# Kernel tuning notes

Measured on AMD Instinct MI355X. Metric: run time of the kernel, lower is better.

Reference implementation:

```python
import jax, jax.numpy as jnp
import numpy as np

N, D, NUM_CLASSES = 8192, 128, 128
ALPHA = 1.0
K = 16


def setup_inputs() -> dict:
    key = jax.random.key(0)
    k1, k2 = jax.random.split(key)
    inputs = jax.random.normal(k1, (N, D), dtype=jnp.float32)
    targets = jax.random.randint(k2, (N,), 0, NUM_CLASSES, dtype=jnp.int64)
    return {"inputs": inputs, "targets": targets}


def knn_softmax(inputs, targets, alpha=ALPHA, k=K):
    n = inputs.shape[0]
    # pairwise euclidean distances (GEMM-based), clamped like the original
    sq = jnp.sum(inputs * inputs, axis=1)                      # [n]
    d2 = sq[:, None] + sq[None, :] - 2.0 * (inputs @ inputs.T)  # [n,n]
    dist = jnp.sqrt(jnp.maximum(d2, 1e-12))

    eye = jnp.eye(n, dtype=bool)
    same = targets[:, None] == targets[None, :]
    pos_mask = same & ~eye          # same label, off-diagonal
    neg_mask = ~same                # different label (diagonal excluded automatically)

    # per-row threshold: (K+1)-th smallest off-diagonal distance
    dm = jnp.where(eye, jnp.inf, dist)
    neg_topk, _ = jax.lax.top_k(-dm, k + 1)   # k+1 smallest (negated)
    thr = -neg_topk[:, k]                      # [n]

    below = dist < thr[:, None]
    pos_sel = pos_mask & below
    neg_sel = neg_mask & below

    exp_d = jnp.exp(-alpha * dist)
    pos_logit = jnp.sum(jnp.where(pos_sel, exp_d, 0.0), axis=1)  # [n]
    neg_logit = jnp.sum(jnp.where(neg_sel, exp_d, 0.0), axis=1)  # [n]
    count_pos = jnp.sum(pos_sel, axis=1)
    count_neg = jnp.sum(neg_sel, axis=1)

    # fallback when no positive falls below the threshold: use the first positive pair
    first_pos = jnp.argmax(pos_mask, axis=1)                     # [n]
    fb_dist = jnp.take_along_axis(dist, first_pos[:, None], axis=1)[:, 0]
    fallback = jnp.exp(-alpha * fb_dist)
    pos_eff = jnp.where(count_pos == 0, fallback, pos_logit)

    # rows with no positives or no negatives at all are skipped (`continue`)
    valid = pos_mask.any(axis=1) & neg_mask.any(axis=1)

    loss_i = -jnp.log(pos_eff / (pos_eff + neg_logit))
    loss = jnp.sum(jnp.where(valid, loss_i, 0.0)) / n

    count_pos_acc = jnp.where(count_pos == 0, 1, count_pos)  # fallback gives len 1
    accuracy = jnp.sum((valid & (count_pos_acc > count_neg)).astype(jnp.float32)) / n
    tp = jnp.sum(jnp.where(valid, count_pos, 0)).astype(jnp.float32) / n
    tn = jnp.sum(jnp.where(valid, count_neg, 0)).astype(jnp.float32) / n
    return loss, accuracy, tp, tn


def reference(inputs, targets):
    return knn_softmax(inputs, targets)
```

## Files before the change

kernel.cpp:

```cpp
#include <hip/hip_runtime.h>

#define NPTS 8192
#define DIM 128
#define NCLS 128
#define KSEL 17
#define RB   64
#define NT8  64
#define CAPW 40
#define SEG  32
#define NSEG 8
#define MBLK 1024
#define BIG 3.0e38f

typedef short bf16x8 __attribute__((ext_vector_type(8)));
typedef float f32x4 __attribute__((ext_vector_type(4)));

__device__ __forceinline__ unsigned short f2bf(float f) {
  unsigned int u = __float_as_uint(f);
  u += 0x7fffu + ((u >> 16) & 1u);
  return (unsigned short)(u >> 16);
}

__device__ __forceinline__ unsigned flipF(float f) {
  unsigned u = __float_as_uint(f);
  return (u & 0x80000000u) ? ~u : (u | 0x80000000u);
}
__device__ __forceinline__ float unflipF(unsigned k) {
  unsigned u = (k & 0x80000000u) ? (k & 0x7fffffffu) : ~k;
  return __uint_as_float(u);
}

__device__ __forceinline__ float kth17_4(float a, float b, float c, float d) {
  const unsigned ka = flipF(a), kb = flipF(b), kc = flipF(c), kd = flipF(d);
  unsigned ans = 0x80000000u;
  for (int bit = 30; bit >= 0; --bit) {
    unsigned mid = ans | (1u << bit);
    int cc = __popcll(__ballot(ka < mid)) + __popcll(__ballot(kb < mid)) +
             __popcll(__ballot(kc < mid)) + __popcll(__ballot(kd < mid));
    if (cc < KSEL) ans = mid;
  }
  return unflipF(ans);
}

__global__ void prep(const float* __restrict__ X, const long long* __restrict__ targets,
                     unsigned short* __restrict__ Xb, float* __restrict__ sqv,
                     int* __restrict__ tgt, int* __restrict__ ccount,
                     int* __restrict__ j0a, int* __restrict__ j1a) {
  const int tid = threadIdx.x;
  if (blockIdx.x == 2048) {
    __shared__ int cc[NCLS], c0[NCLS], c1[NCLS];
    if (tid < NCLS) { cc[tid] = 0; c0[tid] = 0x7fffffff; c1[tid] = 0x7fffffff; }
    __syncthreads();
    for (int base = tid * 4; base < NPTS; base += 1024) {
      const long long* p = targets + base;
#pragma unroll
      for (int k = 0; k < 4; k++) {
        int c = (int)p[k];
        tgt[base + k] = c;
        atomicAdd(&cc[c], 1);
        atomicMin(&c0[c], base + k);
      }
    }
    __syncthreads();
    for (int base = tid * 4; base < NPTS; base += 1024) {
#pragma unroll
      for (int k = 0; k < 4; k++) {
        int c = tgt[base + k];
        if (base + k != c0[c]) atomicMin(&c1[c], base + k);
      }
    }
    __syncthreads();
    if (tid < NCLS) { ccount[tid] = cc[tid]; j0a[tid] = c0[tid]; j1a[tid] = c1[tid]; }
    return;
  }
  const int w = tid >> 6, lane = tid & 63;
  const int gw = blockIdx.x * 4 + w;
  const float* xr = X + (size_t)gw * DIM;
  float a = xr[lane], b = xr[lane + 64];
  Xb[(size_t)gw * DIM + lane] = f2bf(a);
  Xb[(size_t)gw * DIM + lane + 64] = f2bf(b);
  float s = a * a + b * b;
#pragma unroll
  for (int off = 32; off; off >>= 1) s += __shfl_xor(s, off);
  if (lane == 0) sqv[gw] = s;
}

__global__ __launch_bounds__(256, 4) void knn_main(
    const unsigned short* __restrict__ Xb, const float* __restrict__ sqv,
    const int* __restrict__ tgt, float* __restrict__ scr, int* __restrict__ cscr) {
  __shared__ __align__(16) unsigned short shB[2][2048];
  __shared__ __align__(16) float shPub[RB * 64];
  __shared__ int cntL[RB];

  const int tid = threadIdx.x;
  const int w = tid >> 6;
  const int lane = tid & 63;
  const int quad = lane >> 4;
  const int l16 = lane & 15;
  const int rg = blockIdx.x >> 3;
  const int eighth = blockIdx.x & 7;
  const int rbase = rg * RB;
  const int cbase = eighth * 1024;

  const int swoff = (tid << 4) ^ (((tid >> 4) & 7) << 4);
  const unsigned lmlt = (1u << l16) - 1;
  int rdoff[4];
#pragma unroll
  for (int kb = 0; kb < 4; kb++)
    rdoff[kb] = (l16 * 256 + quad * 16 + kb * 64) ^ ((l16 & 7) << 4);

  bf16x8 afrag[4];
  {
    const unsigned short* arow = Xb + (size_t)(rbase + w * 16 + l16) * DIM + quad * 8;
#pragma unroll
    for (int kb = 0; kb < 4; kb++) afrag[kb] = *(const bf16x8*)(arow + kb * 32);
  }
  float sqi[4]; int ti[4];
#pragma unroll
  for (int r = 0; r < 4; r++) {
    int rr = rbase + w * 16 + quad * 4 + r;
    sqi[r] = sqv[rr]; ti[r] = tgt[rr];
  }
  int tdw;
  {
    int d = rbase + w * 16 - cbase;
    tdw = (d >= 0 && d < 1024) ? (d >> 4) : -1;
  }

  const unsigned short* gtile0 = Xb + (size_t)cbase * DIM;
  const float* sqp = sqv + cbase + l16;
  const int*   tgp = tgt + cbase + l16;

  float m1[4], m2[4], m3[4], m4[4];
#pragma unroll
  for (int r = 0; r < 4; r++) { m1[r] = BIG; m2[r] = BIG; m3[r] = BIG; m4[r] = BIG; }
  {
    bf16x8 s0 = *(const bf16x8*)(gtile0 + tid * 8);
    *(bf16x8*)((char*)&shB[0][0] + swoff) = s0;
  }
  float sqc = sqp[0];
  __syncthreads();
  for (int t = 0; t < NT8; t++) {
    const int tn = (t + 1) & (NT8 - 1);
    bf16x8 stg = *(const bf16x8*)(gtile0 + (size_t)tn * 2048 + tid * 8);
    const float sqn = sqp[tn * 16];
    const char* lb = (const char*)&shB[t & 1][0];
    bf16x8 b[4];
#pragma unroll
    for (int kb = 0; kb < 4; kb++) b[kb] = *(const bf16x8*)(lb + rdoff[kb]);
    f32x4 acc = {0.f, 0.f, 0.f, 0.f};
#pragma unroll
    for (int kb = 0; kb < 4; kb++)
      acc = __builtin_amdgcn_mfma_f32_16x16x32_bf16(afrag[kb], b[kb], acc, 0, 0, 0);
    float v[4];
#pragma unroll
    for (int r = 0; r < 4; r++) v[r] = fmaf(-2.0f, acc[r], sqc);
    if (t == tdw) {
#pragma unroll
      for (int r = 0; r < 4; r++) if (l16 == quad * 4 + r) v[r] = BIG;
    }
#pragma unroll
    for (int r = 0; r < 4; r++) {
      m4[r] = fminf(m4[r], fmaxf(m3[r], v[r]));
      m3[r] = fminf(m3[r], fmaxf(m2[r], v[r]));
      m2[r] = fminf(m2[r], fmaxf(m1[r], v[r]));
      m1[r] = fminf(m1[r], v[r]);
    }
    sqc = sqn;
    *(bf16x8*)((char*)&shB[(t & 1) ^ 1][0] + swoff) = stg;
    __syncthreads();
  }

#pragma unroll
  for (int r = 0; r < 4; r++) {
    f32x4 mq = {m1[r], m2[r], m3[r], m4[r]};
    *(f32x4*)&shPub[(w * 16 + quad * 4 + r) * 64 + l16 * 4] = mq;
  }
  __syncthreads();
  float Ur[4] = {0.f, 0.f, 0.f, 0.f};
  for (int rp = 0; rp < 16; rp += 2) {
    const unsigned ka = flipF(shPub[(w * 16 + rp) * 64 + lane]);
    const unsigned kb2 = flipF(shPub[(w * 16 + rp + 1) * 64 + lane]);
    unsigned ansA = 0u, ansB = 0u;
    for (int bit = 31; bit >= 14; --bit) {
      const unsigned mA = ansA | (1u << bit), mB = ansB | (1u << bit);
      const int ca = __popcll(__ballot(ka < mA));
      const int cb = __popcll(__ballot(kb2 < mB));
      if (ca < KSEL) ansA = mA;
      if (cb < KSEL) ansB = mB;
    }
    const float ua = unflipF(ansA | 0x3FFFu), ub = unflipF(ansB | 0x3FFFu);
#pragma unroll
    for (int r = 0; r < 4; r++) {
      const int myrow = quad * 4 + r;
      if (myrow == rp) Ur[r] = ua;
      if (myrow == rp + 1) Ur[r] = ub;
    }
  }

  float* bufD = shPub;
  int cntr[4] = {0, 0, 0, 0};
  {
    bf16x8 s0 = *(const bf16x8*)(gtile0 + tid * 8);
    *(bf16x8*)((char*)&shB[0][0] + swoff) = s0;
  }
  sqc = sqp[0];
  int tjc = tgp[0];
  __syncthreads();
  for (int t = 0; t < NT8; t++) {
    const int tn = (t + 1) & (NT8 - 1);
    bf16x8 stg = *(const bf16x8*)(gtile0 + (size_t)tn * 2048 + tid * 8);
    const float sqn = sqp[tn * 16];
    const int tjn = tgp[tn * 16];
    const char* lb = (const char*)&shB[t & 1][0];
    bf16x8 b[4];
#pragma unroll
    for (int kb = 0; kb < 4; kb++) b[kb] = *(const bf16x8*)(lb + rdoff[kb]);
    f32x4 acc = {0.f, 0.f, 0.f, 0.f};
#pragma unroll
    for (int kb = 0; kb < 4; kb++)
      acc = __builtin_amdgcn_mfma_f32_16x16x32_bf16(afrag[kb], b[kb], acc, 0, 0, 0);
    float v[4];
#pragma unroll
    for (int r = 0; r < 4; r++) v[r] = fmaf(-2.0f, acc[r], sqc);
    if (t == tdw) {
#pragma unroll
      for (int r = 0; r < 4; r++) if (l16 == quad * 4 + r) v[r] = BIG;
    }
#pragma unroll
    for (int r = 0; r < 4; r++) {
      const bool pred = (v[r] <= Ur[r]);
      const unsigned long long bal = __ballot(pred);
      if (bal) {
        const unsigned qm = (unsigned)(bal >> (quad << 4)) & 0xFFFFu;
        const int pos = cntr[r] + __popc(qm & lmlt);
        if (pred && pos < CAPW) {
          unsigned enc = __float_as_uint(fmaxf(v[r] + sqi[r], 0.0f));
          if (tjc == ti[r]) enc |= 0x80000000u;
          bufD[(w * 16 + quad * 4 + r) * CAPW + pos] = __uint_as_float(enc);
        }
        cntr[r] += __popc(qm);
      }
    }
    sqc = sqn; tjc = tjn;
    *(bf16x8*)((char*)&shB[(t & 1) ^ 1][0] + swoff) = stg;
    __syncthreads();
  }
#pragma unroll
  for (int r = 0; r < 4; r++)
    if (l16 == 0) cntL[w * 16 + quad * 4 + r] = cntr[r];
  __syncthreads();

  for (int rl = 0; rl < 16; rl++) {
    const int grow = rbase + w * 16 + rl;
    const int tot = cntL[w * 16 + rl];
    float* srow = scr + (size_t)grow * (NSEG * SEG) + eighth * SEG;
    if (tot <= SEG) {
      if (lane < tot) srow[lane] = bufD[(w * 16 + rl) * CAPW + lane];
      if (lane == 0) cscr[grow * NSEG + eighth] = tot;
    } else {
      const int n = min(tot, CAPW);
      float e = BIG; int m = 0;
      if (lane < n) {
        unsigned u = __float_as_uint(bufD[(w * 16 + rl) * CAPW + lane]);
        m = (int)(u >> 31); e = __uint_as_float(u & 0x7fffffffu);
      }
      for (int round = 0; round < KSEL; round++) {
        float vv = e; int idx = lane;
#pragma unroll
        for (int off = 32; off; off >>= 1) {
          float ov = __shfl_xor(vv, off);
          int   oi = __shfl_xor(idx, off);
          if (ov < vv || (ov == vv && oi < idx)) { vv = ov; idx = oi; }
        }
        if (idx == lane) {
          unsigned ub = __float_as_uint(e);
          if (m) ub |= 0x80000000u;
          srow[round] = __uint_as_float(ub);
          e = BIG;
        }
      }
      if (lane == 0) cscr[grow * NSEG + eighth] = KSEL;
    }
  }
}

__global__ __launch_bounds__(256) void knn_merge(
    const float* __restrict__ scr, const int* __restrict__ cscr,
    const float* __restrict__ sqv, const int* __restrict__ tgt,
    const int* __restrict__ ccount, const int* __restrict__ j0a,
    const int* __restrict__ j1a, const float* __restrict__ X32,
    float* __restrict__ pacc) {
  __shared__ float blockAcc[4];
  const int tid = threadIdx.x;
  const int w = tid >> 6;
  const int lane = tid & 63;
  if (tid < 4) blockAcc[tid] = 0.0f;
  __syncthreads();
  for (int ri = 0; ri < 2; ri++) {
    const int grow = blockIdx.x * 8 + w * 2 + ri;
    const float* srow = scr + (size_t)grow * (NSEG * SEG);
    const int h = lane >> 5, li = lane & 31;
    float e[4]; int mm[4];
#pragma unroll
    for (int j = 0; j < 4; j++) {
      const int seg = j * 2 + h;
      const int cj = cscr[grow * NSEG + seg];
      if (li < cj) {
        unsigned u = __float_as_uint(srow[seg * SEG + li]);
        mm[j] = (int)(u >> 31); e[j] = __uint_as_float(u & 0x7fffffffu);
      } else { e[j] = BIG; mm[j] = 0; }
    }
    const float t17 = kth17_4(e[0], e[1], e[2], e[3]);
    float pls = 0.0f, nls = 0.0f; int cp = 0, cn = 0;
#pragma unroll
    for (int j = 0; j < 4; j++) {
      const bool s = (e[j] < t17);
      const float x = s ? expf(-sqrtf(fmaxf(e[j], 1e-12f))) : 0.0f;
      if (mm[j]) { pls += x; cp += (int)s; }
      else       { nls += x; cn += (int)s; }
    }
    int cpn = cp * 65536 + cn;
#pragma unroll
    for (int off = 32; off; off >>= 1) {
      pls += __shfl_xor(pls, off); nls += __shfl_xor(nls, off);
      cpn += __shfl_xor(cpn, off);
    }
    const int cpt = cpn >> 16, cnt_ = cpn & 0xffff;
    const int c = tgt[grow];
    const int ncl = ccount[c];
    const bool valid = (ncl > 1) && (ncl < NPTS);
    if (valid) {
      float pos_eff;
      if (cpt == 0) {
        const int jf = (grow == j0a[c]) ? j1a[c] : j0a[c];
        const float* xi = X32 + (size_t)grow * DIM;
        const float* xj = X32 + (size_t)jf * DIM;
        float pp = xi[lane] * xj[lane] + xi[lane + 64] * xj[lane + 64];
#pragma unroll
        for (int off = 32; off; off >>= 1) pp += __shfl_xor(pp, off);
        const float fb2 = sqv[grow] + sqv[jf] - 2.0f * pp;
        pos_eff = expf(-sqrtf(fmaxf(fb2, 1e-12f)));
      } else {
        pos_eff = pls;
      }
      if (lane == 0) {
        const float loss_i = -logf(pos_eff / (pos_eff + nls));
        const int cpa = (cpt == 0) ? 1 : cpt;
        atomicAdd(&blockAcc[0], loss_i);
        atomicAdd(&blockAcc[1], (cpa > cnt_) ? 1.0f : 0.0f);
        atomicAdd(&blockAcc[2], (float)cpt);
        atomicAdd(&blockAcc[3], (float)cnt_);
      }
    }
  }
  __syncthreads();
  if (tid < 4) pacc[blockIdx.x * 4 + tid] = blockAcc[tid];
}

__global__ void fin(const float* __restrict__ pacc, float* __restrict__ out) {
  __shared__ float red[256];
  const int tid = threadIdx.x;
  const int c = tid & 3, b0 = tid >> 2;
  float s = 0.0f;
  for (int b = b0; b < MBLK; b += 64) s += pacc[b * 4 + c];
  red[tid] = s;
  __syncthreads();
  if (tid < 4) {
    float t = 0.0f;
    for (int i = tid; i < 256; i += 4) t += red[i];
    out[tid] = t * (1.0f / (float)NPTS);
  }
}

extern "C" void kernel_launch(void* const* d_in, const int* in_sizes, int n_in,
                              void* d_out, int out_size, void* d_ws, size_t ws_size,
                              hipStream_t stream) {
  const float* X = (const float*)d_in[0];
  const long long* targets = (const long long*)d_in[1];
  float* out = (float*)d_out;

  char* ws = (char*)d_ws;
  unsigned short* Xb = (unsigned short*)ws;
  float* sqv    = (float*)   (ws + (2u << 20));
  int*   tgt    = (int*)     (ws + (2u << 20) + (32u << 10));
  int*   ccount = (int*)     (ws + (2u << 20) + (64u << 10));
  int*   j0a    = (int*)     (ws + (2u << 20) + (65u << 10));
  int*   j1a    = (int*)     (ws + (2u << 20) + (66u << 10));
  float* pacc   = (float*)   (ws + (2u << 20) + (68u << 10));
  float* scr = (float*)(ws + (2u << 20) + (128u << 10));
  int* cscr  = (int*)  (ws + (2u << 20) + (128u << 10) +
                        (size_t)NPTS * NSEG * SEG * 4);

  prep<<<2049, 256, 0, stream>>>(X, targets, Xb, sqv, tgt, ccount, j0a, j1a);
  knn_main<<<1024, 256, 0, stream>>>(Xb, sqv, tgt, scr, cscr);
  knn_merge<<<MBLK, 256, 0, stream>>>(scr, cscr, sqv, tgt, ccount, j0a, j1a, X, pacc);
  fin<<<1, 256, 0, stream>>>(pacc, out);
}
```

Measured before the change: 187.3 us.

## Process two column tiles per iteration and keep top-2 per lane

Both passes now stage 32 columns per iteration instead of 16, running two independent MFMA chains per iteration and halving the barrier count. The per-lane running minimum list shrinks from four to two entries, and the threshold search uses 32 candidates per row instead of 64, which cuts register and shared-memory use. Keeping only two candidates per lane per eighth weakens the guarantee that the 17-th smallest upper bound stays valid when several near neighbors land in the same lane. That could alter the threshold or the candidate overflow behavior.

```diff
diff --git a/kernel.cpp b/kernel.cpp
--- a/kernel.cpp
+++ b/kernel.cpp
@@ -5,7 +5,7 @@
 #define NCLS 128
 #define KSEL 17
 #define RB   64
-#define NT8  64
+#define NIT  32
 #define CAPW 40
 #define SEG  32
 #define NSEG 8
@@ -88,8 +88,8 @@
 __global__ __launch_bounds__(256, 4) void knn_main(
     const unsigned short* __restrict__ Xb, const float* __restrict__ sqv,
     const int* __restrict__ tgt, float* __restrict__ scr, int* __restrict__ cscr) {
-  __shared__ __align__(16) unsigned short shB[2][2048];
-  __shared__ __align__(16) float shPub[RB * 64];
+  __shared__ __align__(16) unsigned short shB[2][4096];
+  __shared__ __align__(16) float shPub[RB * CAPW];
   __shared__ int cntL[RB];
 
   const int tid = threadIdx.x;
@@ -102,7 +102,7 @@
   const int rbase = rg * RB;
   const int cbase = eighth * 1024;
 
-  const int swoff = (tid << 4) ^ (((tid >> 4) & 7) << 4);
+  const int w0off = (tid << 5) ^ (((tid >> 3) & 7) << 4);
   const unsigned lmlt = (1u << l16) - 1;
   int rdoff[4];
 #pragma unroll
@@ -131,56 +131,75 @@
   const float* sqp = sqv + cbase + l16;
   const int*   tgp = tgt + cbase + l16;
 
-  float m1[4], m2[4], m3[4], m4[4];
-#pragma unroll
-  for (int r = 0; r < 4; r++) { m1[r] = BIG; m2[r] = BIG; m3[r] = BIG; m4[r] = BIG; }
+  float m1[4], m2[4];
+#pragma unroll
+  for (int r = 0; r < 4; r++) { m1[r] = BIG; m2[r] = BIG; }
   {
-    bf16x8 s0 = *(const bf16x8*)(gtile0 + tid * 8);
-    *(bf16x8*)((char*)&shB[0][0] + swoff) = s0;
-  }
-  float sqc = sqp[0];
-  __syncthreads();
-  for (int t = 0; t < NT8; t++) {
-    const int tn = (t + 1) & (NT8 - 1);
-    bf16x8 stg = *(const bf16x8*)(gtile0 + (size_t)tn * 2048 + tid * 8);
-    const float sqn = sqp[tn * 16];
-    const char* lb = (const char*)&shB[t & 1][0];
-    bf16x8 b[4];
-#pragma unroll
-    for (int kb = 0; kb < 4; kb++) b[kb] = *(const bf16x8*)(lb + rdoff[kb]);
-    f32x4 acc = {0.f, 0.f, 0.f, 0.f};
-#pragma unroll
-    for (int kb = 0; kb < 4; kb++)
-      acc = __builtin_amdgcn_mfma_f32_16x16x32_bf16(afrag[kb], b[kb], acc, 0, 0, 0);
-    float v[4];
-#pragma unroll
-    for (int r = 0; r < 4; r++) v[r] = fmaf(-2.0f, acc[r], sqc);
-    if (t == tdw) {
-#pragma unroll
-      for (int r = 0; r < 4; r++) if (l16 == quad * 4 + r) v[r] = BIG;
-    }
+    bf16x8 s0 = *(const bf16x8*)(gtile0 + tid * 16);
+    bf16x8 s1 = *(const bf16x8*)(gtile0 + tid * 16 + 8);
+    *(bf16x8*)((char*)&shB[0][0] + w0off) = s0;
+    *(bf16x8*)((char*)&shB[0][0] + (w0off ^ 16)) = s1;
+  }
+  float sq0 = sqp[0], sq1 = sqp[16];
+  __syncthreads();
+  for (int j = 0; j < NIT; j++) {
+    const int jn = (j + 1) & (NIT - 1);
+    const unsigned short* src = gtile0 + (size_t)jn * 4096;
+    bf16x8 s0 = *(const bf16x8*)(src + tid * 16);
+    bf16x8 s1 = *(const bf16x8*)(src + tid * 16 + 8);
+    const float nsq0 = sqp[jn * 32], nsq1 = sqp[jn * 32 + 16];
+    const char* lb = (const char*)&shB[j & 1][0];
+    bf16x8 b0[4], b1[4];
+#pragma unroll
+    for (int kb = 0; kb < 4; kb++) {
+      b0[kb] = *(const bf16x8*)(lb + rdoff[kb]);
+      b1[kb] = *(const bf16x8*)(lb + rdoff[kb] + 4096);
+    }
+    f32x4 a0 = {0.f, 0.f, 0.f, 0.f}, a1 = {0.f, 0.f, 0.f, 0.f};
+#pragma unroll
+    for (int kb = 0; kb < 4; kb++) {
+      a0 = __builtin_amdgcn_mfma_f32_16x16x32_bf16(afrag[kb], b0[kb], a0, 0, 0, 0);
+      a1 = __builtin_amdgcn_mfma_f32_16x16x32_bf16(afrag[kb], b1[kb], a1, 0, 0, 0);
+    }
+    float v0[4], v1[4];
 #pragma unroll
     for (int r = 0; r < 4; r++) {
-      m4[r] = fminf(m4[r], fmaxf(m3[r], v[r]));
-      m3[r] = fminf(m3[r], fmaxf(m2[r], v[r]));
-      m2[r] = fminf(m2[r], fmaxf(m1[r], v[r]));
-      m1[r] = fminf(m1[r], v[r]);
-    }
-    sqc = sqn;
-    *(bf16x8*)((char*)&shB[(t & 1) ^ 1][0] + swoff) = stg;
+      v0[r] = fmaf(-2.0f, a0[r], sq0);
+      v1[r] = fmaf(-2.0f, a1[r], sq1);
+    }
+    if ((unsigned)(tdw - 2 * j) < 2u) {
+#pragma unroll
+      for (int r = 0; r < 4; r++) {
+        if (2 * j == tdw && l16 == quad * 4 + r) v0[r] = BIG;
+        if (2 * j + 1 == tdw && l16 == quad * 4 + r) v1[r] = BIG;
+      }
+    }
+#pragma unroll
+    for (int r = 0; r < 4; r++) {
+      m2[r] = fminf(m2[r], fmaxf(m1[r], v0[r]));
+      m1[r] = fminf(m1[r], v0[r]);
+      m2[r] = fminf(m2[r], fmaxf(m1[r], v1[r]));
+      m1[r] = fminf(m1[r], v1[r]);
+    }
+    sq0 = nsq0; sq1 = nsq1;
+    char* wb = (char*)&shB[(j & 1) ^ 1][0];
+    *(bf16x8*)(wb + w0off) = s0;
+    *(bf16x8*)(wb + (w0off ^ 16)) = s1;
     __syncthreads();
   }
 
 #pragma unroll
   for (int r = 0; r < 4; r++) {
-    f32x4 mq = {m1[r], m2[r], m3[r], m4[r]};
-    *(f32x4*)&shPub[(w * 16 + quad * 4 + r) * 64 + l16 * 4] = mq;
+    const int row = w * 16 + quad * 4 + r;
+    shPub[row * 32 + l16 * 2] = m1[r];
+    shPub[row * 32 + l16 * 2 + 1] = m2[r];
   }
   __syncthreads();
   float Ur[4] = {0.f, 0.f, 0.f, 0.f};
   for (int rp = 0; rp < 16; rp += 2) {
-    const unsigned ka = flipF(shPub[(w * 16 + rp) * 64 + lane]);
-    const unsigned kb2 = flipF(shPub[(w * 16 + rp + 1) * 64 + lane]);
+    const int li = lane & 31;
+    const unsigned ka = (lane < 32) ? flipF(shPub[(w * 16 + rp) * 32 + li]) : 0xFFFFFFFFu;
+    const unsigned kb2 = (lane < 32) ? flipF(shPub[(w * 16 + rp + 1) * 32 + li]) : 0xFFFFFFFFu;
     unsigned ansA = 0u, ansB = 0u;
     for (int bit = 31; bit >= 14; --bit) {
       const unsigned mA = ansA | (1u << bit), mB = ansB | (1u << bit);
@@ -201,49 +220,82 @@
   float* bufD = shPub;
   int cntr[4] = {0, 0, 0, 0};
   {
-    bf16x8 s0 = *(const bf16x8*)(gtile0 + tid * 8);
-    *(bf16x8*)((char*)&shB[0][0] + swoff) = s0;
-  }
-  sqc = sqp[0];
-  int tjc = tgp[0];
-  __syncthreads();
-  for (int t = 0; t < NT8; t++) {
-    const int tn = (t + 1) & (NT8 - 1);
-    bf16x8 stg = *(const bf16x8*)(gtile0 + (size_t)tn * 2048 + tid * 8);
-    const float sqn = sqp[tn * 16];
-    const int tjn = tgp[tn * 16];
-    const char* lb = (const char*)&shB[t & 1][0];
-    bf16x8 b[4];
-#pragma unroll
-    for (int kb = 0; kb < 4; kb++) b[kb] = *(const bf16x8*)(lb + rdoff[kb]);
-    f32x4 acc = {0.f, 0.f, 0.f, 0.f};
-#pragma unroll
-    for (int kb = 0; kb < 4; kb++)
-      acc = __builtin_amdgcn_mfma_f32_16x16x32_bf16(afrag[kb], b[kb], acc, 0, 0, 0);
-    float v[4];
-#pragma unroll
-    for (int r = 0; r < 4; r++) v[r] = fmaf(-2.0f, acc[r], sqc);
-    if (t == tdw) {
-#pragma unroll
-      for (int r = 0; r < 4; r++) if (l16 == quad * 4 + r) v[r] = BIG;
-    }
+    bf16x8 s0 = *(const bf16x8*)(gtile0 + tid * 16);
+    bf16x8 s1 = *(const bf16x8*)(gtile0 + tid * 16 + 8);
+    *(bf16x8*)((char*)&shB[0][0] + w0off) = s0;
+    *(bf16x8*)((char*)&shB[0][0] + (w0off ^ 16)) = s1;
+  }
+  sq0 = sqp[0]; sq1 = sqp[16];
+  int tj0 = tgp[0], tj1 = tgp[16];
+  __syncthreads();
+  for (int j = 0; j < NIT; j++) {
+    const int jn = (j + 1) & (NIT - 1);
+    const unsigned short* src = gtile0 + (size_t)jn * 4096;
+    bf16x8 s0 = *(const bf16x8*)(src + tid * 16);
+    bf16x8 s1 = *(const bf16x8*)(src + tid * 16 + 8);
+    const float nsq0 = sqp[jn * 32], nsq1 = sqp[jn * 32 + 16];
+    const int ntj0 = tgp[jn * 32], ntj1 = tgp[jn * 32 + 16];
+    const char* lb = (const char*)&shB[j & 1][0];
+    bf16x8 b0[4], b1[4];
+#pragma unroll
+    for (int kb = 0; kb < 4; kb++) {
+      b0[kb] = *(const bf16x8*)(lb + rdoff[kb]);
+      b1[kb] = *(const bf16x8*)(lb + rdoff[kb] + 4096);
+    }
+    f32x4 a0 = {0.f, 0.f, 0.f, 0.f}, a1 = {0.f, 0.f, 0.f, 0.f};
+#pragma unroll
+    for (int kb = 0; kb < 4; kb++) {
+      a0 = __builtin_amdgcn_mfma_f32_16x16x32_bf16(afrag[kb], b0[kb], a0, 0, 0, 0);
+      a1 = __builtin_amdgcn_mfma_f32_16x16x32_bf16(afrag[kb], b1[kb], a1, 0, 0, 0);
+    }
+    float v0[4], v1[4];
 #pragma unroll
     for (int r = 0; r < 4; r++) {
-      const bool pred = (v[r] <= Ur[r]);
-      const unsigned long long bal = __ballot(pred);
-      if (bal) {
-        const unsigned qm = (unsigned)(bal >> (quad << 4)) & 0xFFFFu;
-        const int pos = cntr[r] + __popc(qm & lmlt);
-        if (pred && pos < CAPW) {
-          unsigned enc = __float_as_uint(fmaxf(v[r] + sqi[r], 0.0f));
-          if (tjc == ti[r]) enc |= 0x80000000u;
-          bufD[(w * 16 + quad * 4 + r) * CAPW + pos] = __uint_as_float(enc);
+      v0[r] = fmaf(-2.0f, a0[r], sq0);
+      v1[r] = fmaf(-2.0f, a1[r], sq1);
+    }
+    if ((unsigned)(tdw - 2 * j) < 2u) {
+#pragma unroll
+      for (int r = 0; r < 4; r++) {
+        if (2 * j == tdw && l16 == quad * 4 + r) v0[r] = BIG;
+        if (2 * j + 1 == tdw && l16 == quad * 4 + r) v1[r] = BIG;
+      }
+    }
+#pragma unroll
+    for (int r = 0; r < 4; r++) {
+      {
+        const bool p = (v0[r] <= Ur[r]);
+        const unsigned long long bal = __ballot(p);
+        if (bal) {
+          const unsigned qm = (unsigned)(bal >> (quad << 4)) & 0xFFFFu;
+          const int pos = cntr[r] + __popc(qm & lmlt);
+          if (p && pos < CAPW) {
+            unsigned enc = __float_as_uint(fmaxf(v0[r] + sqi[r], 0.0f));
+            if (tj0 == ti[r]) enc |= 0x80000000u;
+            bufD[(w * 16 + quad * 4 + r) * CAPW + pos] = __uint_as_float(enc);
+          }
+          cntr[r] += __popc(qm);
         }
-        cntr[r] += __popc(qm);
-      }
-    }
-    sqc = sqn; tjc = tjn;
-    *(bf16x8*)((char*)&shB[(t & 1) ^ 1][0] + swoff) = stg;
+      }
+      {
+        const bool p = (v1[r] <= Ur[r]);
+        const unsigned long long bal = __ballot(p);
+        if (bal) {
+          const unsigned qm = (unsigned)(bal >> (quad << 4)) & 0xFFFFu;
+          const int pos = cntr[r] + __popc(qm & lmlt);
+          if (p && pos < CAPW) {
+            unsigned enc = __float_as_uint(fmaxf(v1[r] + sqi[r], 0.0f));
+            if (tj1 == ti[r]) enc |= 0x80000000u;
+            bufD[(w * 16 + quad * 4 + r) * CAPW + pos] = __uint_as_float(enc);
+          }
+          cntr[r] += __popc(qm);
+        }
+      }
+    }
+    sq0 = nsq0; sq1 = nsq1; tj0 = ntj0; tj1 = ntj1;
+    char* wb = (char*)&shB[(j & 1) ^ 1][0];
+    *(bf16x8*)(wb + w0off) = s0;
+    *(bf16x8*)(wb + (w0off ^ 16)) = s1;
     __syncthreads();
   }
 #pragma unroll
```

Result: faster. 174.1 us (-7.0%).
